# Kernel optimization log

Hardware: AMD Instinct MI355X
Metric: run time of the kernel (lower is better)

Reference implementation:

```python
import jax, jax.numpy as jnp
import numpy as np

CACHE_SIZE = 500_000
TEACHER_DIM = 512
STUDENT_DIM = 128
N_TASKS = 8
BATCH = 16384


def setup_inputs() -> dict:
    key = jax.random.key(0)
    k1, k2, k3, k4, k5 = jax.random.split(key, 5)
    return {
        # GPU-resident KV-cache of precomputed teacher outputs (dict -> dense table)
        "cache_emb": jax.random.normal(k1, (CACHE_SIZE, TEACHER_DIM), dtype=jnp.float32),
        "cache_logits": jax.random.normal(k2, (CACHE_SIZE, N_TASKS), dtype=jnp.float32),
        # nn.Linear(teacher_dim, student_dim, bias=False) weight (stored as in-dim x out-dim)
        "W": (jax.random.normal(k3, (TEACHER_DIM, STUDENT_DIM), dtype=jnp.float32)
              / np.float32(np.sqrt(TEACHER_DIM))),
        # per-query cache slot (result of hashing (user_id, item_id) keys)
        "slot_idx": jax.random.randint(k4, (BATCH,), 0, CACHE_SIZE, dtype=jnp.int32),
        # True = cache hit, False = miss (TTL-expired / unseen) -> zero placeholder
        "hit_mask": jax.random.randint(k5, (BATCH,), 0, 2, dtype=jnp.int32).astype(bool),
    }


def reference(cache_emb, cache_logits, W, slot_idx, hit_mask):
    # query(): gather teacher embeddings/logits per key, zeros on miss, then project.
    hit = hit_mask[:, None]
    emb = jnp.where(hit, cache_emb[slot_idx], 0.0)          # (B, teacher_dim)
    teacher_feats = emb @ W                                  # (B, student_dim)
    teacher_logits = jnp.where(hit, cache_logits[slot_idx], 0.0)  # (B, n_tasks)
    return teacher_feats, teacher_logits
```

## Files before the change

kernel.cpp:

```cpp
#include <hip/hip_runtime.h>

#define TD 512
#define SD 128
#define NT 8
#define BATCH 16384
#define KC 128

typedef float f32x4 __attribute__((ext_vector_type(4)));
typedef short s16x8 __attribute__((ext_vector_type(8)));

__device__ inline unsigned short f2bf_rne(float f) {
    unsigned int u = __builtin_bit_cast(unsigned int, f);
    unsigned int r = u + 0x7fffu + ((u >> 16) & 1u);
    return (unsigned short)(r >> 16);
}

__global__ __launch_bounds__(256) void fused_kernel(
    const float* __restrict__ emb,
    const float* __restrict__ clogits,
    const float* __restrict__ W,
    const int* __restrict__ slot,
    const int* __restrict__ hit,
    float* __restrict__ feats_out,
    float* __restrict__ logits_out)
{
    __shared__ unsigned short Wt[SD * KC];

    const int tid = threadIdx.x;
    const int m0b = blockIdx.x * 64;

    #pragma unroll
    for (int i = 0; i < 2; ++i) {
        int e = i * 256 + tid;
        int row = m0b + (e >> 3);
        int j = e & 7;
        float v = 0.f;
        if (hit[row]) v = clogits[(long)slot[row] * NT + j];
        logits_out[(long)row * NT + j] = v;
    }

    const int wave = tid >> 6;
    const int lane = tid & 63;
    const int lr = lane & 15;
    const int kb = lane >> 4;
    const int m0 = m0b + wave * 16;

    const int arow_idx = m0 + lr;
    const long myslot = slot[arow_idx];
    const bool myhit = hit[arow_idx] != 0;
    const float* arow = emb + myslot * (long)TD;

    const int sn  = tid & 127;
    const int skg = tid >> 7;

    f32x4 acc[8];
    #pragma unroll
    for (int t = 0; t < 8; ++t) acc[t] = (f32x4){0.f, 0.f, 0.f, 0.f};

    char* const wt_base = (char*)&Wt[0];

    for (int chunk = 0; chunk < 4; ++chunk) {
        const int kc0 = chunk * KC;

        f32x4 af[8];
        if (myhit) {
            #pragma unroll
            for (int ks = 0; ks < 4; ++ks) {
                const int kgo = kc0 + ks * 32 + kb * 8;
                af[2 * ks]     = *(const f32x4*)(arow + kgo);
                af[2 * ks + 1] = *(const f32x4*)(arow + kgo + 4);
            }
        }

        __syncthreads();

        #pragma unroll
        for (int q = 0; q < 16; ++q) {
            const int kl = skg * 64 + q * 4;
            const int kg = kc0 + kl;
            unsigned short b4[4];
            #pragma unroll
            for (int ii = 0; ii < 4; ++ii)
                b4[ii] = f2bf_rne(W[(long)(kg + ii) * SD + sn]);
            const int byte_off = ((sn * KC + kl) * 2) ^ ((sn & 7) << 4);
            *(unsigned long long*)(wt_base + byte_off) =
                __builtin_bit_cast(unsigned long long,
                    (ushort4){b4[0], b4[1], b4[2], b4[3]});
        }

        __syncthreads();

        #pragma unroll
        for (int ks = 0; ks < 4; ++ks) {
            s16x8 a;
            if (myhit) {
                const f32x4 f0 = af[2 * ks];
                const f32x4 f1 = af[2 * ks + 1];
                #pragma unroll
                for (int j = 0; j < 4; ++j) a[j]     = (short)f2bf_rne(f0[j]);
                #pragma unroll
                for (int j = 0; j < 4; ++j) a[4 + j] = (short)f2bf_rne(f1[j]);
            } else {
                a = (s16x8){0, 0, 0, 0, 0, 0, 0, 0};
            }
            const int klo = ks * 32 + kb * 8;
            #pragma unroll
            for (int t = 0; t < 8; ++t) {
                const int n = t * 16 + lr;
                const int boff = ((n * KC + klo) * 2) ^ ((n & 7) << 4);
                const s16x8 b = *(const s16x8*)(wt_base + boff);
                acc[t] = __builtin_amdgcn_mfma_f32_16x16x32_bf16(a, b, acc[t], 0, 0, 0);
            }
        }
    }

    #pragma unroll
    for (int t = 0; t < 8; ++t) {
        #pragma unroll
        for (int r = 0; r < 4; ++r) {
            const int orow = m0 + kb * 4 + r;
            const int ocol = t * 16 + lr;
            feats_out[(long)orow * SD + ocol] = acc[t][r];
        }
    }
}

extern "C" void kernel_launch(void* const* d_in, const int* in_sizes, int n_in,
                              void* d_out, int out_size, void* d_ws, size_t ws_size,
                              hipStream_t stream) {
    const float* cache_emb    = (const float*)d_in[0];
    const float* cache_logits = (const float*)d_in[1];
    const float* W            = (const float*)d_in[2];
    const int*   slot_idx     = (const int*)d_in[3];
    const int*   hitm         = (const int*)d_in[4];

    float* feats_out  = (float*)d_out;
    float* logits_out = (float*)d_out + (long)BATCH * SD;

    fused_kernel<<<BATCH / 64, 256, 0, stream>>>(cache_emb, cache_logits, W,
                                                 slot_idx, hitm,
                                                 feats_out, logits_out);
}
```

Measured before the change: 18.44 us.

## Pre-transpose W to bf16 once and split K across waves with LDS reduction

Adds a small prep kernel that converts W to a transposed bf16 copy in workspace, so blocks no longer each convert and stage W through shared memory. The main kernel now handles 16 rows per block, with each of its 4 waves covering a quarter of K. B fragments are read straight from global/L2, and the partial sums are reduced through LDS, which lets the output be written with vectorized stores. This gives 4x more blocks and more parallel gather latency, at the cost of a second launch and repeated L2 reads of W by every block.

```diff
diff --git a/kernel.cpp b/kernel.cpp
--- a/kernel.cpp
+++ b/kernel.cpp
@@ -1,128 +1,116 @@
 #include <hip/hip_runtime.h>
+#include <hip/hip_bf16.h>
 
 #define TD 512
 #define SD 128
 #define NT 8
 #define BATCH 16384
-#define KC 128
 
 typedef float f32x4 __attribute__((ext_vector_type(4)));
 typedef short s16x8 __attribute__((ext_vector_type(8)));
 
-__device__ inline unsigned short f2bf_rne(float f) {
-    unsigned int u = __builtin_bit_cast(unsigned int, f);
-    unsigned int r = u + 0x7fffu + ((u >> 16) & 1u);
-    return (unsigned short)(r >> 16);
+__device__ inline unsigned short f2bf(float f) {
+    __hip_bfloat16 h = __float2bfloat16(f);
+    return __builtin_bit_cast(unsigned short, h);
+}
+
+__global__ __launch_bounds__(256) void wprep_kernel(
+    const float* __restrict__ W, unsigned short* __restrict__ Wt) {
+    int tid = blockIdx.x * 256 + threadIdx.x;
+    int n = tid >> 9;
+    int k = tid & 511;
+    Wt[tid] = f2bf(W[k * SD + n]);
 }
 
 __global__ __launch_bounds__(256) void fused_kernel(
     const float* __restrict__ emb,
     const float* __restrict__ clogits,
-    const float* __restrict__ W,
+    const unsigned short* __restrict__ Wt,
     const int* __restrict__ slot,
     const int* __restrict__ hit,
     float* __restrict__ feats_out,
     float* __restrict__ logits_out)
 {
-    __shared__ unsigned short Wt[SD * KC];
+    __shared__ float red[4][16][SD];
 
     const int tid = threadIdx.x;
-    const int m0b = blockIdx.x * 64;
+    const int m0 = blockIdx.x * 16;
 
-    #pragma unroll
-    for (int i = 0; i < 2; ++i) {
-        int e = i * 256 + tid;
-        int row = m0b + (e >> 3);
-        int j = e & 7;
+    if (tid < 128) {
+        const int row = m0 + (tid >> 3);
+        const int j = tid & 7;
         float v = 0.f;
         if (hit[row]) v = clogits[(long)slot[row] * NT + j];
         logits_out[(long)row * NT + j] = v;
     }
 
-    const int wave = tid >> 6;
+    const int w    = tid >> 6;
     const int lane = tid & 63;
-    const int lr = lane & 15;
-    const int kb = lane >> 4;
-    const int m0 = m0b + wave * 16;
+    const int lr   = lane & 15;
+    const int kb   = lane >> 4;
+    const int kbase = w * 128;
 
     const int arow_idx = m0 + lr;
     const long myslot = slot[arow_idx];
     const bool myhit = hit[arow_idx] != 0;
-    const float* arow = emb + myslot * (long)TD;
+    const float* arow = emb + myslot * (long)TD + kbase;
 
-    const int sn  = tid & 127;
-    const int skg = tid >> 7;
+    f32x4 af[8];
+    if (myhit) {
+        #pragma unroll
+        for (int ks = 0; ks < 4; ++ks) {
+            const int ko = ks * 32 + kb * 8;
+            af[2 * ks]     = *(const f32x4*)(arow + ko);
+            af[2 * ks + 1] = *(const f32x4*)(arow + ko + 4);
+        }
+    }
 
     f32x4 acc[8];
     #pragma unroll
     for (int t = 0; t < 8; ++t) acc[t] = (f32x4){0.f, 0.f, 0.f, 0.f};
 
-    char* const wt_base = (char*)&Wt[0];
+    const unsigned short* wtb = Wt + kbase + kb * 8;
 
-    for (int chunk = 0; chunk < 4; ++chunk) {
-        const int kc0 = chunk * KC;
-
-        f32x4 af[8];
+    #pragma unroll
+    for (int ks = 0; ks < 4; ++ks) {
+        s16x8 a;
         if (myhit) {
+            const f32x4 f0 = af[2 * ks];
+            const f32x4 f1 = af[2 * ks + 1];
             #pragma unroll
-            for (int ks = 0; ks < 4; ++ks) {
-                const int kgo = kc0 + ks * 32 + kb * 8;
-                af[2 * ks]     = *(const f32x4*)(arow + kgo);
-                af[2 * ks + 1] = *(const f32x4*)(arow + kgo + 4);
-            }
+            for (int j = 0; j < 4; ++j) a[j]     = (short)f2bf(f0[j]);
+            #pragma unroll
+            for (int j = 0; j < 4; ++j) a[4 + j] = (short)f2bf(f1[j]);
+        } else {
+            a = (s16x8){0, 0, 0, 0, 0, 0, 0, 0};
         }
-
-        __syncthreads();
-
         #pragma unroll
-        for (int q = 0; q < 16; ++q) {
-            const int kl = skg * 64 + q * 4;
-            const int kg = kc0 + kl;
-            unsigned short b4[4];
-            #pragma unroll
-            for (int ii = 0; ii < 4; ++ii)
-                b4[ii] = f2bf_rne(W[(long)(kg + ii) * SD + sn]);
-            const int byte_off = ((sn * KC + kl) * 2) ^ ((sn & 7) << 4);
-            *(unsigned long long*)(wt_base + byte_off) =
-                __builtin_bit_cast(unsigned long long,
-                    (ushort4){b4[0], b4[1], b4[2], b4[3]});
-        }
-
-        __syncthreads();
-
-        #pragma unroll
-        for (int ks = 0; ks < 4; ++ks) {
-            s16x8 a;
-            if (myhit) {
-                const f32x4 f0 = af[2 * ks];
-                const f32x4 f1 = af[2 * ks + 1];
-                #pragma unroll
-                for (int j = 0; j < 4; ++j) a[j]     = (short)f2bf_rne(f0[j]);
-                #pragma unroll
-                for (int j = 0; j < 4; ++j) a[4 + j] = (short)f2bf_rne(f1[j]);
-            } else {
-                a = (s16x8){0, 0, 0, 0, 0, 0, 0, 0};
-            }
-            const int klo = ks * 32 + kb * 8;
-            #pragma unroll
-            for (int t = 0; t < 8; ++t) {
-                const int n = t * 16 + lr;
-                const int boff = ((n * KC + klo) * 2) ^ ((n & 7) << 4);
-                const s16x8 b = *(const s16x8*)(wt_base + boff);
-                acc[t] = __builtin_amdgcn_mfma_f32_16x16x32_bf16(a, b, acc[t], 0, 0, 0);
-            }
+        for (int t = 0; t < 8; ++t) {
+            const s16x8 b = *(const s16x8*)(wtb + (t * 16 + lr) * TD + ks * 32);
+            acc[t] = __builtin_amdgcn_mfma_f32_16x16x32_bf16(a, b, acc[t], 0, 0, 0);
         }
     }
 
     #pragma unroll
     for (int t = 0; t < 8; ++t) {
         #pragma unroll
-        for (int r = 0; r < 4; ++r) {
-            const int orow = m0 + kb * 4 + r;
-            const int ocol = t * 16 + lr;
-            feats_out[(long)orow * SD + ocol] = acc[t][r];
-        }
+        for (int i = 0; i < 4; ++i)
+            red[w][kb * 4 + i][t * 16 + lr] = acc[t][i];
     }
+    __syncthreads();
+
+    const int row = tid >> 4;
+    const int cg  = (tid & 15) * 8;
+    f32x4 s0 = (f32x4){0.f, 0.f, 0.f, 0.f};
+    f32x4 s1 = (f32x4){0.f, 0.f, 0.f, 0.f};
+    #pragma unroll
+    for (int w2 = 0; w2 < 4; ++w2) {
+        s0 += *(const f32x4*)&red[w2][row][cg];
+        s1 += *(const f32x4*)&red[w2][row][cg + 4];
+    }
+    float* o = feats_out + (long)(m0 + row) * SD + cg;
+    *(f32x4*)o       = s0;
+    *(f32x4*)(o + 4) = s1;
 }
 
 extern "C" void kernel_launch(void* const* d_in, const int* in_sizes, int n_in,
@@ -137,7 +125,10 @@
     float* feats_out  = (float*)d_out;
     float* logits_out = (float*)d_out + (long)BATCH * SD;
 
-    fused_kernel<<<BATCH / 64, 256, 0, stream>>>(cache_emb, cache_logits, W,
+    unsigned short* Wt = (unsigned short*)d_ws;
+
+    wprep_kernel<<<256, 256, 0, stream>>>(W, Wt);
+    fused_kernel<<<BATCH / 16, 256, 0, stream>>>(cache_emb, cache_logits, Wt,
                                                  slot_idx, hitm,
                                                  feats_out, logits_out);
 }
```

Result: slower. 29.32 us (+59.1%).
